# Performance work log

Hardware: AMD Instinct MI355X
Metric: run time of the kernel (lower is better)

## Reference

```python
import jax, jax.numpy as jnp
import numpy as np

BSZ, SLEN, DIN = 4, 2048, 1024
EMB, HNO = 1024, 16
HSZ = EMB // HNO


def setup_inputs() -> dict:
    key = jax.random.key(0)
    ks = jax.random.split(key, 7)
    s = 1.0 / np.sqrt(DIN)
    return {
        "x": jax.random.normal(ks[0], (BSZ, SLEN, DIN), dtype=jnp.float32),
        "Wq": jax.random.uniform(ks[1], (EMB, DIN), jnp.float32, -s, s),
        "bq": jax.random.uniform(ks[2], (EMB,), jnp.float32, -s, s),
        "Wk": jax.random.uniform(ks[3], (EMB, DIN), jnp.float32, -s, s),
        "bk": jax.random.uniform(ks[4], (EMB,), jnp.float32, -s, s),
        "Wv": jax.random.uniform(ks[5], (EMB, DIN), jnp.float32, -s, s),
        "bv": jax.random.uniform(ks[6], (EMB,), jnp.float32, -s, s),
    }


def reference(x, Wq, bq, Wk, bk, Wv, bv):
    bsz, slen, _ = x.shape
    # QKV projections, split heads: [b, h, s, hd]
    def proj(W, b):
        y = jnp.einsum('bsd,ed->bse', x, W) + b
        return y.reshape(bsz, slen, HNO, HSZ).transpose(0, 2, 1, 3)
    q, k, v = proj(Wq, bq), proj(Wk, bk), proj(Wv, bv)
    # scaled causal attention scores [b, h, s, s]
    scores = jnp.einsum('bhqd,bhkd->bhqk', q, k) / jnp.sqrt(jnp.asarray(HSZ, x.dtype))
    causal = jnp.tril(jnp.ones((slen, slen), dtype=bool))
    scores = jnp.where(causal[None, None], scores, -jnp.inf)
    attn = jax.nn.softmax(scores, axis=-1)
    value = jnp.einsum('bhqk,bhkd->bhqd', attn, v)  # [b, h, s, hd]
    # faithful to source: swap (s, hd) THEN flatten to [b, s, emb]
    value = jnp.swapaxes(value, -2, -1).reshape(bsz, slen, -1)
    return value
```

## Files before the change

kernel.cpp:

```cpp
#include <hip/hip_runtime.h>


#define BSZ 4
#define SLEN 2048
#define DIN 1024
#define EMB 1024
#define HNO 16
#define HSZ 64

typedef unsigned short u16;
typedef __bf16 bf16x8_t __attribute__((ext_vector_type(8)));
typedef float f32x4_t __attribute__((ext_vector_type(4)));

__device__ __forceinline__ u16 f2bf(float f) {
    unsigned u = __float_as_uint(f);
    u += 0x7FFFu + ((u >> 16) & 1u);
    return (u16)(u >> 16);
}

__device__ __forceinline__ float exp2_fast(float x) {
    float r;
    asm("v_exp_f32 %0, %1" : "=v"(r) : "v"(x));
    return r;
}

__device__ __forceinline__ unsigned cvt_pk_bf16(float lo, float hi) {
    unsigned r;
    asm("v_cvt_pk_bf16_f32 %0, %1, %2" : "=v"(r) : "v"(lo), "v"(hi));
    return r;
}

__device__ __forceinline__ void gld16(void* lds, const void* g) {
    __builtin_amdgcn_global_load_lds(
        (const __attribute__((address_space(1))) void*)g,
        (__attribute__((address_space(3))) void*)lds, 16, 0, 0);
}

#define VMW0()                                                                 \
    do {                                                                       \
        asm volatile("s_waitcnt vmcnt(0)" ::: "memory");                       \
        __builtin_amdgcn_sched_barrier(0);                                     \
    } while (0)

__global__ __launch_bounds__(256) void cvt_bf16_kernel(
    const float* __restrict__ x,  const float* __restrict__ wq,
    const float* __restrict__ wk, const float* __restrict__ wv,
    u16* __restrict__ xo, u16* __restrict__ wo)
{
    const int y = blockIdx.y;
    const float* src = (y == 0) ? x : (y == 1) ? wq : (y == 2) ? wk : wv;
    u16* dst = (y == 0) ? xo : wo + (size_t)(y - 1) * (EMB * DIN);
    const int n8 = (y == 0) ? (BSZ * SLEN * DIN / 8) : (EMB * DIN / 8);

    for (int i = blockIdx.x * 256 + threadIdx.x; i < n8; i += gridDim.x * 256) {
        float4 a = *reinterpret_cast<const float4*>(src + (size_t)i * 8);
        float4 b = *reinterpret_cast<const float4*>(src + (size_t)i * 8 + 4);
        union { u16 h[8]; uint4 u; } p;
        p.h[0] = f2bf(a.x); p.h[1] = f2bf(a.y); p.h[2] = f2bf(a.z); p.h[3] = f2bf(a.w);
        p.h[4] = f2bf(b.x); p.h[5] = f2bf(b.y); p.h[6] = f2bf(b.z); p.h[7] = f2bf(b.w);
        *reinterpret_cast<uint4*>(dst + (size_t)i * 8) = p.u;
    }
}

__global__ __launch_bounds__(256, 3) void qkv_gemm_kernel(
    const u16* __restrict__ xb, const u16* __restrict__ wb,
    const float* __restrict__ bq, const float* __restrict__ bk,
    const float* __restrict__ bv,
    u16* __restrict__ qkv, u16* __restrict__ vt)
{
    __shared__ __attribute__((aligned(16))) u16 SH[2 * 128 * 64];
    u16* AsF = SH;
    u16* BsF = SH + 128 * 64;

    const int t    = threadIdx.x;
    const int wid  = t >> 6;
    const int lane = t & 63;
    const int g    = lane >> 4;
    const int r16  = lane & 15;
    const int wm   = wid >> 1, wn = wid & 1;

    const int wg = blockIdx.x;
    const int x  = wg & 7;
    const int j  = wg >> 3;
    const int bx  = (x & 3) * 16 + (j & 15);
    const int byn = (x >> 2) * 12 + (j >> 4);
    const int m0  = bx * 128;
    const int n0g = byn * 128;

    const int rowoff = t >> 3;
    const int colswz = ((t & 7) ^ (rowoff & 7)) * 8;
    const u16* srcA = xb + (size_t)(m0 + rowoff) * DIN + colswz;
    const u16* srcB = wb + (size_t)(n0g + rowoff) * DIN + colswz;

    const int s0 = (g ^ (r16 & 7)) * 8;

    f32x4_t acc[4][4] = {};

#pragma unroll 1
    for (int kt = 0; kt < 16; ++kt) {
        __syncthreads();
#pragma unroll
        for (int u = 0; u < 4; ++u) {
            gld16(AsF + u * 2048 + t * 8,
                  srcA + (size_t)u * 32 * DIN + kt * 64);
            gld16(BsF + u * 2048 + t * 8,
                  srcB + (size_t)u * 32 * DIN + kt * 64);
        }
        __syncthreads();

        bf16x8_t af[4], bfv[4];
#pragma unroll
        for (int i2 = 0; i2 < 4; ++i2) {
            af[i2]  = *reinterpret_cast<const bf16x8_t*>(
                AsF + (wm * 64 + i2 * 16 + r16) * 64 + s0);
            bfv[i2] = *reinterpret_cast<const bf16x8_t*>(
                BsF + (wn * 64 + i2 * 16 + r16) * 64 + s0);
        }
#pragma unroll
        for (int i2 = 0; i2 < 4; ++i2)
#pragma unroll
            for (int j2 = 0; j2 < 4; ++j2)
                acc[i2][j2] = __builtin_amdgcn_mfma_f32_16x16x32_bf16(
                    af[i2], bfv[j2], acc[i2][j2], 0, 0, 0);
#pragma unroll
        for (int i2 = 0; i2 < 4; ++i2) {
            af[i2]  = *reinterpret_cast<const bf16x8_t*>(
                AsF + (wm * 64 + i2 * 16 + r16) * 64 + (s0 ^ 32));
            bfv[i2] = *reinterpret_cast<const bf16x8_t*>(
                BsF + (wn * 64 + i2 * 16 + r16) * 64 + (s0 ^ 32));
        }
#pragma unroll
        for (int i2 = 0; i2 < 4; ++i2)
#pragma unroll
            for (int j2 = 0; j2 < 4; ++j2)
                acc[i2][j2] = __builtin_amdgcn_mfma_f32_16x16x32_bf16(
                    af[i2], bfv[j2], acc[i2][j2], 0, 0, 0);
    }

    const size_t per = (size_t)BSZ * HNO * SLEN * HSZ;
    const bool isV = (n0g >= 2 * 1024);
    u16* lout = SH;
    const int b  = m0 >> 11;
    const int sB = m0 & 2047;
#pragma unroll
    for (int h = 0; h < 2; ++h) {
        __syncthreads();
        if (!isV) {
            if (wm == h) {
#pragma unroll
                for (int j2 = 0; j2 < 4; ++j2) {
                    const int el  = wn * 64 + j2 * 16 + r16;
                    const int egl = n0g + el;
                    const int mat = egl >> 10;
                    const int e   = egl & 1023;
                    const float bval = (mat == 0) ? bq[e] : bk[e];
                    const float qsv  = (mat == 0) ? 0.125f * 1.44269504f : 1.0f;
#pragma unroll
                    for (int i2 = 0; i2 < 4; ++i2)
#pragma unroll
                        for (int r = 0; r < 4; ++r) {
                            int ml = i2 * 16 + g * 4 + r;
                            lout[ml * 136 + el] =
                                f2bf((acc[i2][j2][r] + bval) * qsv);
                        }
                }
            }
            __syncthreads();
#pragma unroll
            for (int it = 0; it < 4; ++it) {
                int cid = it * 256 + t;
                int row = cid >> 4;
                int cc  = cid & 15;
                int egl = n0g + cc * 8;
                int mat = egl >> 10;
                int e   = egl & 1023;
                int s   = sB + h * 64 + row;
                uint4 v = *reinterpret_cast<const uint4*>(&lout[row * 136 + cc * 8]);
                *reinterpret_cast<uint4*>(qkv + (size_t)mat * per +
                    ((((size_t)b * HNO) + (e >> 6)) * SLEN + s) * HSZ + (e & 63)) = v;
            }
        } else {
            if (wm == h) {
#pragma unroll
                for (int j2 = 0; j2 < 4; ++j2) {
                    const int el  = wn * 64 + j2 * 16 + r16;
                    const int e   = (n0g + el) & 1023;
                    const float bval = bv[e];
#pragma unroll
                    for (int i2 = 0; i2 < 4; ++i2)
#pragma unroll
                        for (int r = 0; r < 4; ++r) {
                            int ml = i2 * 16 + g * 4 + r;
                            lout[el * 66 + ml] = f2bf(acc[i2][j2][r] + bval);
                        }
                }
            }
            __syncthreads();
#pragma unroll
            for (int it = 0; it < 4; ++it) {
                int cid  = it * 256 + t;
                int el   = cid >> 3;
                int sgrp = (cid & 7) * 8;
                int egl  = n0g + el;
                int hh   = (egl >> 6) & 15;
                int d    = egl & 63;
                int s    = sB + h * 64 + sgrp;
                uint4 v = *reinterpret_cast<const uint4*>(&lout[el * 66 + sgrp]);
                *reinterpret_cast<uint4*>(vt +
                    (((size_t)(b * HNO + hh)) * HSZ + d) * SLEN + s) = v;
            }
        }
    }
}

__global__ __launch_bounds__(512, 6) void attn_kernel(
    const u16* __restrict__ qb, const u16* __restrict__ kb,
    const u16* __restrict__ vtg, float* __restrict__ out)
{
    __shared__ __attribute__((aligned(16))) u16 Ks[2][64][64];
    __shared__ __attribute__((aligned(16))) u16 Vt[2][64][64];
    __shared__ __attribute__((aligned(16))) u16 P2[8][16][72];

    const int t    = threadIdx.x;
    const int wid  = t >> 6;
    const int lane = t & 63;
    const int g    = lane >> 4;
    const int r16  = lane & 15;
    const int r8   = r16 & 7;

    const int w   = blockIdx.x;
    const int idx = w >> 3;
    const int bh  = (w & 7) * 8 + (idx & 7);
    const int qt  = 15 - (idx >> 3);
    const int q0  = qt * 128;
    const size_t base = (size_t)bh * (SLEN * HSZ);

    const int qi = q0 + wid * 16 + r16;
    bf16x8_t qf0 = *reinterpret_cast<const bf16x8_t*>(&qb[base + (size_t)qi * HSZ + g * 8]);
    bf16x8_t qf1 = *reinterpret_cast<const bf16x8_t*>(&qb[base + (size_t)qi * HSZ + 32 + g * 8]);

    const int srow = t >> 3;
    const int schk = ((t & 7) ^ (srow & 7)) * 8;
    const u16* ksrc = kb  + base + (size_t)srow * HSZ + schk;
    const u16* vsrc = vtg + base + (size_t)srow * SLEN + schk;
    const int ldst = wid * 8 * 64;

    f32x4_t o[4] = {};
    float lrow = 0.f;

    const int ntiles = 2 * qt + 2;
    const int qw0 = q0 + wid * 16;
    const int qmax_wave = qw0 + 15;

    gld16(&Ks[0][0][0] + ldst, ksrc);
    gld16(&Vt[0][0][0] + ldst, vsrc);
    VMW0();
    __builtin_amdgcn_s_barrier();

#pragma unroll 1
    for (int kt = 0; kt < ntiles; ++kt) {
        const int kv0  = kt * 64;
        const int bsel = kt & 1;
        if (kt + 1 < ntiles) {
            gld16(&Ks[bsel ^ 1][0][0] + ldst, ksrc + (size_t)(kv0 + 64) * HSZ);
            gld16(&Vt[bsel ^ 1][0][0] + ldst, vsrc + (kv0 + 64));
        }

        if (kv0 <= qmax_wave) {
            const u16* Kb = &Ks[bsel][0][0];
            const u16* Vb = &Vt[bsel][0][0];

            f32x4_t c_[4];
            __builtin_amdgcn_s_setprio(1);
#pragma unroll
            for (int m = 0; m < 4; ++m) {
                bf16x8_t a0 = *reinterpret_cast<const bf16x8_t*>(
                    Kb + (m * 16 + r16) * 64 + (g ^ r8) * 8);
                bf16x8_t a1 = *reinterpret_cast<const bf16x8_t*>(
                    Kb + (m * 16 + r16) * 64 + ((4 + g) ^ r8) * 8);
                f32x4_t cc = {};
                cc = __builtin_amdgcn_mfma_f32_16x16x32_bf16(a0, qf0, cc, 0, 0, 0);
                cc = __builtin_amdgcn_mfma_f32_16x16x32_bf16(a1, qf1, cc, 0, 0, 0);
                c_[m] = cc;
            }
            __builtin_amdgcn_s_setprio(0);

            float p[16];
            if (kv0 + 63 > qw0) {
#pragma unroll
                for (int m = 0; m < 4; ++m)
#pragma unroll
                    for (int r = 0; r < 4; ++r) {
                        int kj = kv0 + m * 16 + g * 4 + r;
                        float sv = (kj <= qi) ? c_[m][r] : -1e30f;
                        p[m * 4 + r] = exp2_fast(sv - 4.0f);
                    }
            } else {
#pragma unroll
                for (int m = 0; m < 4; ++m)
#pragma unroll
                    for (int r = 0; r < 4; ++r)
                        p[m * 4 + r] = exp2_fast(c_[m][r] - 4.0f);
            }
            float y0 = (p[0] + p[1]) + (p[2] + p[3]);
            float y1 = (p[4] + p[5]) + (p[6] + p[7]);
            float y2 = (p[8] + p[9]) + (p[10] + p[11]);
            float y3 = (p[12] + p[13]) + (p[14] + p[15]);
            float tsum = (y0 + y1) + (y2 + y3);
            tsum += __shfl_xor(tsum, 16);
            tsum += __shfl_xor(tsum, 32);
            lrow += tsum;

#pragma unroll
            for (int m = 0; m < 4; ++m) {
                uint2 pk;
                pk.x = cvt_pk_bf16(p[m * 4 + 0], p[m * 4 + 1]);
                pk.y = cvt_pk_bf16(p[m * 4 + 2], p[m * 4 + 3]);
                *reinterpret_cast<uint2*>(&P2[wid][r16][m * 16 + g * 4]) = pk;
            }

            __builtin_amdgcn_s_setprio(1);
#pragma unroll
            for (int c = 0; c < 2; ++c) {
                bf16x8_t pf = *reinterpret_cast<const bf16x8_t*>(
                    &P2[wid][r16][c * 32 + g * 8]);
#pragma unroll
                for (int j2 = 0; j2 < 4; ++j2) {
                    bf16x8_t vf = *reinterpret_cast<const bf16x8_t*>(
                        Vb + (j2 * 16 + r16) * 64 + ((c * 4 + g) ^ r8) * 8);
                    o[j2] = __builtin_amdgcn_mfma_f32_16x16x32_bf16(
                        vf, pf, o[j2], 0, 0, 0);
                }
            }
            __builtin_amdgcn_s_setprio(0);
        }

        VMW0();
        __builtin_amdgcn_s_barrier();
    }

    float rinv = 1.0f / lrow;
    const int b = bh >> 4, h = bh & 15;
    float* outb = out + (size_t)b * (SLEN * EMB) + (size_t)h * (HSZ * SLEN);
#pragma unroll
    for (int j2 = 0; j2 < 4; ++j2) {
#pragma unroll
        for (int r = 0; r < 4; ++r) {
            int d = j2 * 16 + g * 4 + r;
            outb[(size_t)d * SLEN + qi] = o[j2][r] * rinv;
        }
    }
}

extern "C" void kernel_launch(void* const* d_in, const int* in_sizes, int n_in,
                              void* d_out, int out_size, void* d_ws, size_t ws_size,
                              hipStream_t stream) {
    const float* x  = (const float*)d_in[0];
    const float* Wq = (const float*)d_in[1];
    const float* bq = (const float*)d_in[2];
    const float* Wk = (const float*)d_in[3];
    const float* bk = (const float*)d_in[4];
    const float* Wv = (const float*)d_in[5];
    const float* bv = (const float*)d_in[6];
    float* out = (float*)d_out;

    const size_t per = (size_t)BSZ * HNO * SLEN * HSZ;
    u16* qw = (u16*)d_ws;
    u16* kw = qw + per;
    u16* vw = kw + per;

    u16* xb = (u16*)d_out;
    u16* wb = xb + (size_t)BSZ * SLEN * DIN;

    cvt_bf16_kernel<<<dim3(256, 4), 256, 0, stream>>>(x, Wq, Wk, Wv, xb, wb);
    qkv_gemm_kernel<<<1536, 256, 0, stream>>>(xb, wb, bq, bk, bv, qw, vw);
    attn_kernel<<<1024, 512, 0, stream>>>(qw, kw, vw, out);
}
```

Measured before the change: 119.7 us.

## Enlarge QKV GEMM tile to 256x128 with double-buffered A and overlapped loads

The QKV projection GEMM now computes 256x128 tiles per block, so the grid shrinks from 1536 to 768 blocks and each B tile is reused twice as much. The A tile is double-buffered so the next k-step's loads are issued before the MFMAs. The B tile reload is placed between the two k-halves behind an LDS wait and barrier, and MFMA sections run at raised wave priority. The larger accumulator set and LDS footprint drop the occupancy target from 3 to 2 blocks per CU. The V epilogue now uses packed bf16 conversion and a padded 136-stride transpose buffer.

After: 122.2 us. 1.02x slower.

```diff
diff --git a/kernel.cpp b/kernel.cpp
--- a/kernel.cpp
+++ b/kernel.cpp
@@ -39,6 +39,12 @@
 #define VMW0()                                                                 \
     do {                                                                       \
         asm volatile("s_waitcnt vmcnt(0)" ::: "memory");                       \
+        __builtin_amdgcn_sched_barrier(0);                                     \
+    } while (0)
+
+#define LGKM0()                                                                \
+    do {                                                                       \
+        asm volatile("s_waitcnt lgkmcnt(0)" ::: "memory");                     \
         __builtin_amdgcn_sched_barrier(0);                                     \
     } while (0)
 
@@ -62,15 +68,14 @@
     }
 }
 
-__global__ __launch_bounds__(256, 3) void qkv_gemm_kernel(
+__global__ __launch_bounds__(256, 2) void qkv_gemm_kernel(
     const u16* __restrict__ xb, const u16* __restrict__ wb,
     const float* __restrict__ bq, const float* __restrict__ bk,
     const float* __restrict__ bv,
     u16* __restrict__ qkv, u16* __restrict__ vt)
 {
-    __shared__ __attribute__((aligned(16))) u16 SH[2 * 128 * 64];
-    u16* AsF = SH;
-    u16* BsF = SH + 128 * 64;
+    __shared__ __attribute__((aligned(16))) u16 SH[2 * 16384 + 8192];
+    u16* Bs = SH + 2 * 16384;
 
     const int t    = threadIdx.x;
     const int wid  = t >> 6;
@@ -79,13 +84,13 @@
     const int r16  = lane & 15;
     const int wm   = wid >> 1, wn = wid & 1;
 
-    const int wg = blockIdx.x;
-    const int x  = wg & 7;
-    const int j  = wg >> 3;
-    const int bx  = (x & 3) * 16 + (j & 15);
-    const int byn = (x >> 2) * 12 + (j >> 4);
-    const int m0  = bx * 128;
-    const int n0g = byn * 128;
+    const int wg  = blockIdx.x;
+    const int xcd = wg & 7;
+    const int j   = wg >> 3;
+    const int jm  = j / 12;
+    const int jn  = j - jm * 12;
+    const int m0  = ((xcd & 3) * 8 + jm) * 256;
+    const int n0g = ((xcd >> 2) * 12 + jn) * 128;
 
     const int rowoff = t >> 3;
     const int colswz = ((t & 7) ^ (rowoff & 7)) * 8;
@@ -94,47 +99,78 @@
 
     const int s0 = (g ^ (r16 & 7)) * 8;
 
-    f32x4_t acc[4][4] = {};
+    f32x4_t acc[8][4] = {};
+
+#pragma unroll
+    for (int u = 0; u < 8; ++u)
+        gld16(SH + u * 2048 + t * 8, srcA + (size_t)u * 32 * DIN);
+#pragma unroll
+    for (int v = 0; v < 4; ++v)
+        gld16(Bs + v * 2048 + t * 8, srcB + (size_t)v * 32 * DIN);
+    VMW0();
+    __builtin_amdgcn_s_barrier();
 
 #pragma unroll 1
     for (int kt = 0; kt < 16; ++kt) {
-        __syncthreads();
-#pragma unroll
-        for (int u = 0; u < 4; ++u) {
-            gld16(AsF + u * 2048 + t * 8,
-                  srcA + (size_t)u * 32 * DIN + kt * 64);
-            gld16(BsF + u * 2048 + t * 8,
-                  srcB + (size_t)u * 32 * DIN + kt * 64);
-        }
-        __syncthreads();
-
-        bf16x8_t af[4], bfv[4];
-#pragma unroll
-        for (int i2 = 0; i2 < 4; ++i2) {
-            af[i2]  = *reinterpret_cast<const bf16x8_t*>(
-                AsF + (wm * 64 + i2 * 16 + r16) * 64 + s0);
-            bfv[i2] = *reinterpret_cast<const bf16x8_t*>(
-                BsF + (wn * 64 + i2 * 16 + r16) * 64 + s0);
-        }
-#pragma unroll
-        for (int i2 = 0; i2 < 4; ++i2)
+        const bool nl = (kt != 15);
+        const u16* Acur = SH + (kt & 1) * 16384;
+        u16*       Aalt = SH + ((kt + 1) & 1) * 16384;
+
+        if (nl) {
+#pragma unroll
+            for (int u = 0; u < 8; ++u)
+                gld16(Aalt + u * 2048 + t * 8,
+                      srcA + (size_t)u * 32 * DIN + (kt + 1) * 64);
+        }
+
+        bf16x8_t af[8], bf0[4], bf1[4];
+#pragma unroll
+        for (int i2 = 0; i2 < 8; ++i2)
+            af[i2] = *reinterpret_cast<const bf16x8_t*>(
+                Acur + (wm * 128 + i2 * 16 + r16) * 64 + s0);
+#pragma unroll
+        for (int j2 = 0; j2 < 4; ++j2) {
+            bf0[j2] = *reinterpret_cast<const bf16x8_t*>(
+                Bs + (wn * 64 + j2 * 16 + r16) * 64 + s0);
+            bf1[j2] = *reinterpret_cast<const bf16x8_t*>(
+                Bs + (wn * 64 + j2 * 16 + r16) * 64 + (s0 ^ 32));
+        }
+
+        __builtin_amdgcn_s_setprio(1);
+#pragma unroll
+        for (int i2 = 0; i2 < 8; ++i2)
 #pragma unroll
             for (int j2 = 0; j2 < 4; ++j2)
                 acc[i2][j2] = __builtin_amdgcn_mfma_f32_16x16x32_bf16(
-                    af[i2], bfv[j2], acc[i2][j2], 0, 0, 0);
-#pragma unroll
-        for (int i2 = 0; i2 < 4; ++i2) {
-            af[i2]  = *reinterpret_cast<const bf16x8_t*>(
-                AsF + (wm * 64 + i2 * 16 + r16) * 64 + (s0 ^ 32));
-            bfv[i2] = *reinterpret_cast<const bf16x8_t*>(
-                BsF + (wn * 64 + i2 * 16 + r16) * 64 + (s0 ^ 32));
-        }
-#pragma unroll
-        for (int i2 = 0; i2 < 4; ++i2)
+                    af[i2], bf0[j2], acc[i2][j2], 0, 0, 0);
+        __builtin_amdgcn_s_setprio(0);
+
+#pragma unroll
+        for (int i2 = 0; i2 < 8; ++i2)
+            af[i2] = *reinterpret_cast<const bf16x8_t*>(
+                Acur + (wm * 128 + i2 * 16 + r16) * 64 + (s0 ^ 32));
+
+        LGKM0();
+        __builtin_amdgcn_s_barrier();
+
+        if (nl) {
+#pragma unroll
+            for (int v = 0; v < 4; ++v)
+                gld16(Bs + v * 2048 + t * 8,
+                      srcB + (size_t)v * 32 * DIN + (kt + 1) * 64);
+        }
+
+        __builtin_amdgcn_s_setprio(1);
+#pragma unroll
+        for (int i2 = 0; i2 < 8; ++i2)
 #pragma unroll
             for (int j2 = 0; j2 < 4; ++j2)
                 acc[i2][j2] = __builtin_amdgcn_mfma_f32_16x16x32_bf16(
-                    af[i2], bfv[j2], acc[i2][j2], 0, 0, 0);
+                    af[i2], bf1[j2], acc[i2][j2], 0, 0, 0);
+        __builtin_amdgcn_s_setprio(0);
+
+        VMW0();
+        __builtin_amdgcn_s_barrier();
     }
 
     const size_t per = (size_t)BSZ * HNO * SLEN * HSZ;
@@ -142,6 +178,8 @@
     u16* lout = SH;
     const int b  = m0 >> 11;
     const int sB = m0 & 2047;
+    const int mat = n0g >> 10;
+
 #pragma unroll
     for (int h = 0; h < 2; ++h) {
         __syncthreads();
@@ -149,14 +187,12 @@
             if (wm == h) {
 #pragma unroll
                 for (int j2 = 0; j2 < 4; ++j2) {
-                    const int el  = wn * 64 + j2 * 16 + r16;
-                    const int egl = n0g + el;
-                    const int mat = egl >> 10;
-                    const int e   = egl & 1023;
+                    const int el = wn * 64 + j2 * 16 + r16;
+                    const int e  = (n0g + el) & 1023;
                     const float bval = (mat == 0) ? bq[e] : bk[e];
                     const float qsv  = (mat == 0) ? 0.125f * 1.44269504f : 1.0f;
 #pragma unroll
-                    for (int i2 = 0; i2 < 4; ++i2)
+                    for (int i2 = 0; i2 < 8; ++i2)
 #pragma unroll
                         for (int r = 0; r < 4; ++r) {
                             int ml = i2 * 16 + g * 4 + r;
@@ -167,14 +203,12 @@
             }
             __syncthreads();
 #pragma unroll
-            for (int it = 0; it < 4; ++it) {
+            for (int it = 0; it < 8; ++it) {
                 int cid = it * 256 + t;
                 int row = cid >> 4;
                 int cc  = cid & 15;
-                int egl = n0g + cc * 8;
-                int mat = egl >> 10;
-                int e   = egl & 1023;
-                int s   = sB + h * 64 + row;
+                int e   = (n0g + cc * 8) & 1023;
+                int s   = sB + h * 128 + row;
                 uint4 v = *reinterpret_cast<const uint4*>(&lout[row * 136 + cc * 8]);
                 *reinterpret_cast<uint4*>(qkv + (size_t)mat * per +
                     ((((size_t)b * HNO) + (e >> 6)) * SLEN + s) * HSZ + (e & 63)) = v;
@@ -183,29 +217,32 @@
             if (wm == h) {
 #pragma unroll
                 for (int j2 = 0; j2 < 4; ++j2) {
-                    const int el  = wn * 64 + j2 * 16 + r16;
-                    const int e   = (n0g + el) & 1023;
+                    const int el = wn * 64 + j2 * 16 + r16;
+                    const int e  = (n0g + el) & 1023;
                     const float bval = bv[e];
 #pragma unroll
-                    for (int i2 = 0; i2 < 4; ++i2)
-#pragma unroll
-                        for (int r = 0; r < 4; ++r) {
-                            int ml = i2 * 16 + g * 4 + r;
-                            lout[el * 66 + ml] = f2bf(acc[i2][j2][r] + bval);
-                        }
+                    for (int i2 = 0; i2 < 8; ++i2) {
+                        uint2 pk;
+                        pk.x = cvt_pk_bf16(acc[i2][j2][0] + bval,
+                                           acc[i2][j2][1] + bval);
+                        pk.y = cvt_pk_bf16(acc[i2][j2][2] + bval,
+                                           acc[i2][j2][3] + bval);
+                        *reinterpret_cast<uint2*>(
+                            &lout[el * 136 + i2 * 16 + g * 4]) = pk;
+                    }
                 }
             }
             __syncthreads();
 #pragma unroll
-            for (int it = 0; it < 4; ++it) {
-                int cid  = it * 256 + t;
-                int el   = cid >> 3;
-                int sgrp = (cid & 7) * 8;
-                int egl  = n0g + el;
-                int hh   = (egl >> 6) & 15;
-                int d    = egl & 63;
-                int s    = sB + h * 64 + sgrp;
-                uint4 v = *reinterpret_cast<const uint4*>(&lout[el * 66 + sgrp]);
+            for (int it = 0; it < 8; ++it) {
+                int cid = it * 256 + t;
+                int el  = cid >> 4;
+                int sc  = cid & 15;
+                int egl = n0g + el;
+                int hh  = (egl >> 6) & 15;
+                int d   = egl & 63;
+                int s   = sB + h * 128 + sc * 8;
+                uint4 v = *reinterpret_cast<const uint4*>(&lout[el * 136 + sc * 8]);
                 *reinterpret_cast<uint4*>(vt +
                     (((size_t)(b * HNO + hh)) * HSZ + d) * SLEN + s) = v;
             }
@@ -373,6 +410,6 @@
     u16* wb = xb + (size_t)BSZ * SLEN * DIN;
 
     cvt_bf16_kernel<<<dim3(256, 4), 256, 0, stream>>>(x, Wq, Wk, Wv, xb, wb);
-    qkv_gemm_kernel<<<1536, 256, 0, stream>>>(xb, wb, bq, bk, bv, qw, vw);
+    qkv_gemm_kernel<<<768, 256, 0, stream>>>(xb, wb, bq, bk, bv, qw, vw);
     attn_kernel<<<1024, 512, 0, stream>>>(qw, kw, vw, out);
 }
```

## Overlap next K-tile global loads with MFMA in QKV projection GEMM

Applied to the files above, without the earlier changes.

The projection GEMM now preloads the first K tile, then each iteration reads the whole tile's fragments into registers, issues async global-to-LDS loads for the next tile into the same single buffer, and runs the MFMAs while those loads are in flight. Explicit waitcnt, barriers and sched_barriers replace the two __syncthreads per iteration, and s_setprio raises priority during the MFMA block. This hides global load latency behind compute without adding LDS. The cost is doubled fragment register use, which may reduce occupancy.

New measurement: 119.0 us, median of 2. Within noise of the previous version (-0.6%).

```diff
diff --git a/kernel.cpp b/kernel.cpp
--- a/kernel.cpp
+++ b/kernel.cpp
@@ -39,6 +39,12 @@
 #define VMW0()                                                                 \
     do {                                                                       \
         asm volatile("s_waitcnt vmcnt(0)" ::: "memory");                       \
+        __builtin_amdgcn_sched_barrier(0);                                     \
+    } while (0)
+
+#define LGKM0()                                                                \
+    do {                                                                       \
+        asm volatile("s_waitcnt lgkmcnt(0)" ::: "memory");                     \
         __builtin_amdgcn_sched_barrier(0);                                     \
     } while (0)
 
@@ -96,45 +102,57 @@
 
     f32x4_t acc[4][4] = {};
 
+#pragma unroll
+    for (int u = 0; u < 4; ++u) {
+        gld16(AsF + u * 2048 + t * 8, srcA + (size_t)u * 32 * DIN);
+        gld16(BsF + u * 2048 + t * 8, srcB + (size_t)u * 32 * DIN);
+    }
+    VMW0();
+    __builtin_amdgcn_s_barrier();
+
 #pragma unroll 1
     for (int kt = 0; kt < 16; ++kt) {
-        __syncthreads();
-#pragma unroll
-        for (int u = 0; u < 4; ++u) {
-            gld16(AsF + u * 2048 + t * 8,
-                  srcA + (size_t)u * 32 * DIN + kt * 64);
-            gld16(BsF + u * 2048 + t * 8,
-                  srcB + (size_t)u * 32 * DIN + kt * 64);
-        }
-        __syncthreads();
-
-        bf16x8_t af[4], bfv[4];
+        bf16x8_t af[4][2], bfv[4][2];
 #pragma unroll
         for (int i2 = 0; i2 < 4; ++i2) {
-            af[i2]  = *reinterpret_cast<const bf16x8_t*>(
+            af[i2][0] = *reinterpret_cast<const bf16x8_t*>(
                 AsF + (wm * 64 + i2 * 16 + r16) * 64 + s0);
-            bfv[i2] = *reinterpret_cast<const bf16x8_t*>(
+            af[i2][1] = *reinterpret_cast<const bf16x8_t*>(
+                AsF + (wm * 64 + i2 * 16 + r16) * 64 + (s0 ^ 32));
+            bfv[i2][0] = *reinterpret_cast<const bf16x8_t*>(
                 BsF + (wn * 64 + i2 * 16 + r16) * 64 + s0);
-        }
-#pragma unroll
-        for (int i2 = 0; i2 < 4; ++i2)
-#pragma unroll
-            for (int j2 = 0; j2 < 4; ++j2)
-                acc[i2][j2] = __builtin_amdgcn_mfma_f32_16x16x32_bf16(
-                    af[i2], bfv[j2], acc[i2][j2], 0, 0, 0);
-#pragma unroll
-        for (int i2 = 0; i2 < 4; ++i2) {
-            af[i2]  = *reinterpret_cast<const bf16x8_t*>(
-                AsF + (wm * 64 + i2 * 16 + r16) * 64 + (s0 ^ 32));
-            bfv[i2] = *reinterpret_cast<const bf16x8_t*>(
+            bfv[i2][1] = *reinterpret_cast<const bf16x8_t*>(
                 BsF + (wn * 64 + i2 * 16 + r16) * 64 + (s0 ^ 32));
         }
-#pragma unroll
-        for (int i2 = 0; i2 < 4; ++i2)
-#pragma unroll
-            for (int j2 = 0; j2 < 4; ++j2)
-                acc[i2][j2] = __builtin_amdgcn_mfma_f32_16x16x32_bf16(
-                    af[i2], bfv[j2], acc[i2][j2], 0, 0, 0);
+        LGKM0();
+        __builtin_amdgcn_s_barrier();
+        __builtin_amdgcn_sched_barrier(0);
+
+        if (kt != 15) {
+#pragma unroll
+            for (int u = 0; u < 4; ++u) {
+                gld16(AsF + u * 2048 + t * 8,
+                      srcA + (size_t)u * 32 * DIN + (kt + 1) * 64);
+                gld16(BsF + u * 2048 + t * 8,
+                      srcB + (size_t)u * 32 * DIN + (kt + 1) * 64);
+            }
+        }
+        __builtin_amdgcn_sched_barrier(0);
+
+        __builtin_amdgcn_s_setprio(1);
+#pragma unroll
+        for (int kk = 0; kk < 2; ++kk)
+#pragma unroll
+            for (int i2 = 0; i2 < 4; ++i2)
+#pragma unroll
+                for (int j2 = 0; j2 < 4; ++j2)
+                    acc[i2][j2] = __builtin_amdgcn_mfma_f32_16x16x32_bf16(
+                        af[i2][kk], bfv[j2][kk], acc[i2][j2], 0, 0, 0);
+        __builtin_amdgcn_s_setprio(0);
+        __builtin_amdgcn_sched_barrier(0);
+
+        VMW0();
+        __builtin_amdgcn_s_barrier();
     }
 
     const size_t per = (size_t)BSZ * HNO * SLEN * HSZ;
```
